# Kernel optimization log

Hardware: AMD Instinct MI355X
Metric: run time of the kernel (lower is better)

## Reference

```python
import jax, jax.numpy as jnp
import numpy as np

D = 128        # d_model
B = 32         # graphs in batch
NV = 500       # vars per graph -> 2*NV literals per graph
NL = B * 2 * NV            # 32000 literals
NC_G = 2000                # clauses per graph
NC = B * NC_G              # 64000 clauses
K = 3                      # literals per clause
NE = NC * K                # 192000 edges


def setup_inputs() -> dict:
    key = jax.random.key(0)
    ks = jax.random.split(key, 16)
    s = 1.0 / np.sqrt(D)
    inp = {
        'x_unk': jax.random.uniform(ks[0], (NL, D), dtype=jnp.float32),
        'C_w': jax.random.normal(ks[1], (D,), dtype=jnp.float32) * s,
        'C_b': jax.random.normal(ks[2], (D,), dtype=jnp.float32) * s,
        'Wih_lc': jax.random.normal(ks[3], (4 * D, D), dtype=jnp.float32) * s,
        'Whh_lc': jax.random.normal(ks[4], (4 * D, D), dtype=jnp.float32) * s,
        'bih_lc': jax.random.normal(ks[5], (4 * D,), dtype=jnp.float32) * s,
        'bhh_lc': jax.random.normal(ks[6], (4 * D,), dtype=jnp.float32) * s,
        'Wih_cl': jax.random.normal(ks[7], (4 * D, 2 * D), dtype=jnp.float32) * s,
        'Whh_cl': jax.random.normal(ks[8], (4 * D, D), dtype=jnp.float32) * s,
        'bih_cl': jax.random.normal(ks[9], (4 * D,), dtype=jnp.float32) * s,
        'bhh_cl': jax.random.normal(ks[10], (4 * D,), dtype=jnp.float32) * s,
        'out_w': jax.random.normal(ks[11], (D, 1), dtype=jnp.float32) * s,
        'out_b': jax.random.normal(ks[12], (1,), dtype=jnp.float32) * s,
    }
    rng = np.random.default_rng(0)
    # each clause samples K literals within its own graph
    lit_local = rng.integers(0, 2 * NV, size=(B, NC_G, K))
    offs = (np.arange(B) * 2 * NV)[:, None, None]
    inp['lit_idx'] = jnp.asarray((lit_local + offs).reshape(-1), dtype=jnp.int32)
    inp['clause_idx'] = jnp.asarray(np.repeat(np.arange(NC), K), dtype=jnp.int32)
    inp['l_batch'] = jnp.asarray(np.repeat(np.arange(B), 2 * NV), dtype=jnp.int32)
    # literal flip: swap pos/neg halves within each graph
    loc = np.arange(2 * NV)
    flip_local = np.concatenate([loc[NV:], loc[:NV]])
    inp['flip_perm'] = jnp.asarray(((np.arange(B) * 2 * NV)[:, None] + flip_local[None, :]).reshape(-1), dtype=jnp.int32)
    inp['num_iters'] = 4
    return inp


def _lstm_step(x, h, c, Wih, Whh, bih, bhh):
    # PyTorch LSTM cell: gates ordered [i, f, g, o]
    g = x @ Wih.T + h @ Whh.T + (bih + bhh)
    i, f, gg, o = jnp.split(g, 4, axis=-1)
    c2 = jax.nn.sigmoid(f) * c + jax.nn.sigmoid(i) * jnp.tanh(gg)
    h2 = jax.nn.sigmoid(o) * jnp.tanh(c2)
    return h2, c2


def reference(x_unk, C_w, C_b, Wih_lc, Whh_lc, bih_lc, bhh_lc,
              Wih_cl, Whh_cl, bih_cl, bhh_cl, out_w, out_b,
              clause_idx, lit_idx, l_batch, flip_perm, num_iters):
    n_lits = x_unk.shape[0]
    n_clauses = clause_idx.shape[0] // K
    # init embeddings: x_unk ~ U[0,1); x_c = C_init(1) repeated; cell states zero
    h_l, c_l = x_unk, jnp.zeros_like(x_unk)
    h_c = jnp.broadcast_to(C_w + C_b, (n_clauses, D))  # Linear(1,d) on ones(1)
    c_c = jnp.zeros((n_clauses, D), dtype=x_unk.dtype)
    for _ in range(num_iters):
        # lit -> clause: msg = adj_t @ x_l (SpMM via gather+segment_sum)
        msg_c = jax.ops.segment_sum(h_l[lit_idx], clause_idx, num_segments=n_clauses)
        h_c, c_c = _lstm_step(msg_c, h_c, c_c, Wih_lc, Whh_lc, bih_lc, bhh_lc)
        # clause -> lit: msg = adj_t.T @ x_c, concat with flipped literals
        msg_l = jax.ops.segment_sum(h_c[clause_idx], lit_idx, num_segments=n_lits)
        inp = jnp.concatenate([msg_l, h_l[flip_perm]], axis=-1)  # [NL, 2D]
        h_l, c_l = _lstm_step(inp, h_l, c_l, Wih_cl, Whh_cl, bih_cl, bhh_cl)
    votes = h_l @ out_w + out_b  # [NL, 1]
    sums = jax.ops.segment_sum(votes, l_batch, num_segments=B)
    cnts = jax.ops.segment_sum(jnp.ones((n_lits, 1), votes.dtype), l_batch, num_segments=B)
    vote_reduced = sums / cnts  # global_mean_pool
    return vote_reduced, votes, h_l
```

## Files before the change

kernel.cpp:

```cpp
#include <hip/hip_runtime.h>
#include <hip/hip_bf16.h>

#define D     128
#define NLIT  32000
#define NCLA  64000
#define KLIT  3
#define NEDGE 192000
#define BGR   32
#define ITERS 4
#define LITS_PER_GRAPH 1000

typedef _Float16 f16x8 __attribute__((ext_vector_type(8)));
typedef float    f32x4 __attribute__((ext_vector_type(4)));

#define TSTRIDE 40

__device__ __forceinline__ float sigf(float x)  { return 1.f / (1.f + __expf(-x)); }
__device__ __forceinline__ float tanhft(float x){ return 1.f - 2.f / (__expf(2.f * x) + 1.f); }

__global__ void conv_x_kernel(const float* __restrict__ x, _Float16* __restrict__ o) {
    int t = blockIdx.x * blockDim.x + threadIdx.x;
    if (t >= NLIT * 16) return;
    const float* p = x + t * 8;
    f16x8 v;
#pragma unroll
    for (int i = 0; i < 8; ++i) v[i] = (_Float16)p[i];
    *(f16x8*)((_Float16*)o + t * 8) = v;
}

__global__ void conv_wc_kernel(const float* __restrict__ Wih,
                               const float* __restrict__ Whh,
                               _Float16* __restrict__ Wc) {
    int n = blockIdx.x, k = threadIdx.x;
    float v = (k < 128) ? Wih[n * 128 + k] : Whh[n * 128 + k - 128];
    Wc[n * 256 + k] = (_Float16)v;
}

__global__ void conv_wl_kernel(const float* __restrict__ Wih,
                               const float* __restrict__ Whh,
                               _Float16* __restrict__ Wl) {
    int n = blockIdx.x, k = threadIdx.x;
    float v = (k < 256) ? Wih[n * 256 + k] : Whh[n * 128 + k - 256];
    Wl[n * 384 + k] = (_Float16)v;
}

__global__ void conv_bias_kernel(const float* bih_c, const float* bhh_c, float* bc,
                                 const float* bih_l, const float* bhh_l, float* bl,
                                 const float* C_w, const float* C_b,
                                 _Float16* hc0g) {
    int t = threadIdx.x;
    bc[t] = bih_c[t] + bhh_c[t];
    bl[t] = bih_l[t] + bhh_l[t];
    if (t < 128) hc0g[t] = (_Float16)(C_w[t] + C_b[t]);
}

__global__ void count_edges_kernel(const int* __restrict__ lit_idx,
                                   int* __restrict__ counts) {
    int e = blockIdx.x * blockDim.x + threadIdx.x;
    if (e < NEDGE) atomicAdd(&counts[lit_idx[e]], 1);
}

__global__ __launch_bounds__(256)
void block_sum_kernel(const int* __restrict__ counts, int* __restrict__ bsum) {
    int b = blockIdx.x, t = threadIdx.x;
    int v = counts[b * 256 + t];
    int lane = t & 63, w = t >> 6;
#pragma unroll
    for (int off = 32; off > 0; off >>= 1) v += __shfl_down(v, off, 64);
    __shared__ int ws[4];
    if (lane == 0) ws[w] = v;
    __syncthreads();
    if (t == 0) bsum[b] = ws[0] + ws[1] + ws[2] + ws[3];
}

__global__ void scan_bsum_kernel(const int* __restrict__ bsum,
                                 int* __restrict__ ebsum,
                                 int* __restrict__ starts) {
    __shared__ int s[128];
    int t = threadIdx.x;
    int v = (t < 125) ? bsum[t] : 0;
    s[t] = v;
    __syncthreads();
    for (int off = 1; off < 128; off <<= 1) {
        int y = (t >= off) ? s[t - off] : 0;
        __syncthreads();
        s[t] += y;
        __syncthreads();
    }
    if (t < 125) ebsum[t] = s[t] - v;
    if (t == 0) starts[NLIT] = NEDGE;
}

__global__ __launch_bounds__(256)
void scan_write_kernel(const int* __restrict__ counts,
                       const int* __restrict__ ebsum,
                       int* __restrict__ starts,
                       int* __restrict__ cursor) {
    int b = blockIdx.x, t = threadIdx.x;
    int idx = b * 256 + t;
    int v = counts[idx];
    int lane = t & 63, w = t >> 6;
    int x = v;
#pragma unroll
    for (int off = 1; off < 64; off <<= 1) {
        int y = __shfl_up(x, off, 64);
        if (lane >= off) x += y;
    }
    __shared__ int wsum[4];
    if (lane == 63) wsum[w] = x;
    __syncthreads();
    int woff = 0;
#pragma unroll
    for (int i = 0; i < 4; ++i) if (i < w) woff += wsum[i];
    int g = ebsum[b] + woff + x - v;
    starts[idx] = g;
    cursor[idx] = g;
}

__global__ void fill_csr_kernel(const int* __restrict__ lit_idx,
                                const int* __restrict__ clause_idx,
                                int* __restrict__ cursor,
                                int* __restrict__ edge_clause) {
    int e = blockIdx.x * blockDim.x + threadIdx.x;
    if (e < NEDGE) {
        int l = lit_idx[e];
        int pos = atomicAdd(&cursor[l], 1);
        edge_clause[pos] = clause_idx[e];
    }
}

__global__ void gather_msg_kernel(const _Float16* __restrict__ h_c16,
                                  _Float16* __restrict__ msg16,
                                  const int* __restrict__ starts,
                                  const int* __restrict__ edge_clause) {
    int t = blockIdx.x * blockDim.x + threadIdx.x;
    if (t >= NLIT * 16) return;
    int l = t >> 4;
    int off = (t & 15) * 8;
    int s = starts[l], e = starts[l + 1];
    float a[8];
#pragma unroll
    for (int i = 0; i < 8; ++i) a[i] = 0.f;
    for (int j = s; j < e; ++j) {
        f16x8 v = *(const f16x8*)&h_c16[(size_t)edge_clause[j] * D + off];
#pragma unroll
        for (int i = 0; i < 8; ++i) a[i] += (float)v[i];
    }
    f16x8 o;
#pragma unroll
    for (int i = 0; i < 8; ++i) o[i] = (_Float16)a[i];
    *(f16x8*)&msg16[(size_t)l * D + off] = o;
}

__global__ __launch_bounds__(256, 3)
void clause_mfma_kernel(const _Float16* __restrict__ h_l16,
                        const _Float16* __restrict__ h_c_old,
                        _Float16* __restrict__ h_c_new,
                        _Float16* __restrict__ c_c16,
                        const _Float16* __restrict__ Wc,
                        const float* __restrict__ bc,
                        const _Float16* __restrict__ hc0g,
                        const int* __restrict__ lit_idx,
                        int first) {
    __shared__ _Float16 At[2][64 * TSTRIDE];
    __shared__ int      lidx[192];

    const int tid  = threadIdx.x;
    const int w    = tid >> 6;
    const int lane = tid & 63;
    const int qd   = lane >> 4;
    const int ln   = lane & 15;
    const int c    = blockIdx.x & 1;
    const int row0 = (blockIdx.x >> 1) * 64;

    if (tid < 192) lidx[tid] = lit_idx[row0 * 3 + tid];
    __syncthreads();

    const int nrow = c * 64 + 16 * w + ln;
    const int koff = qd * 8;
    const int m    = tid >> 2;
    const int col8 = (tid & 3) * 8;

    const _Float16* p0 = &h_l16[(size_t)lidx[3 * m + 0] * D + col8];
    const _Float16* p1 = &h_l16[(size_t)lidx[3 * m + 1] * D + col8];
    const _Float16* p2 = &h_l16[(size_t)lidx[3 * m + 2] * D + col8];
    const _Float16* pc = &h_c_old[(size_t)(row0 + m) * D + col8];
    const _Float16* pb0 = &Wc[(size_t)(0 * 128 + nrow) * 256 + koff];
    const _Float16* pb1 = &Wc[(size_t)(1 * 128 + nrow) * 256 + koff];
    const _Float16* pb2 = &Wc[(size_t)(2 * 128 + nrow) * 256 + koff];
    const _Float16* pb3 = &Wc[(size_t)(3 * 128 + nrow) * 256 + koff];

    f16x8 ldB0 = *(const f16x8*)pb0; pb0 += 32;
    f16x8 ldB1 = *(const f16x8*)pb1; pb1 += 32;
    f16x8 ldB2 = *(const f16x8*)pb2; pb2 += 32;
    f16x8 ldB3 = *(const f16x8*)pb3; pb3 += 32;
    f16x8 ldG0 = *(const f16x8*)p0;  p0 += 32;
    f16x8 ldG1 = *(const f16x8*)p1;  p1 += 32;
    f16x8 ldG2 = *(const f16x8*)p2;  p2 += 32;

    f32x4 acc[4][4];
#pragma unroll
    for (int R = 0; R < 4; ++R)
#pragma unroll
        for (int g = 0; g < 4; ++g) { acc[R][g][0]=0.f; acc[R][g][1]=0.f; acc[R][g][2]=0.f; acc[R][g][3]=0.f; }

    for (int ch = 0; ch < 8; ++ch) {
        _Float16* buf = (_Float16*)At[ch & 1];
        f16x8 o = (ch < 4) ? (f16x8)(ldG0 + ldG1 + ldG2) : ldG0;
        *(f16x8*)&buf[m * TSTRIDE + col8] = o;
        f16x8 bf0 = ldB0, bf1 = ldB1, bf2 = ldB2, bf3 = ldB3;
        if (ch < 7) {
            ldB0 = *(const f16x8*)pb0; pb0 += 32;
            ldB1 = *(const f16x8*)pb1; pb1 += 32;
            ldB2 = *(const f16x8*)pb2; pb2 += 32;
            ldB3 = *(const f16x8*)pb3; pb3 += 32;
            if (ch + 1 < 4) {
                ldG0 = *(const f16x8*)p0; p0 += 32;
                ldG1 = *(const f16x8*)p1; p1 += 32;
                ldG2 = *(const f16x8*)p2; p2 += 32;
            } else if (first) {
                ldG0 = *(const f16x8*)&hc0g[(ch + 1 - 4) * 32 + col8];
            } else {
                ldG0 = *(const f16x8*)pc; pc += 32;
            }
        }
        __syncthreads();
        f16x8 af[4];
#pragma unroll
        for (int R = 0; R < 4; ++R)
            af[R] = *(const f16x8*)&buf[(16 * R + ln) * TSTRIDE + koff];
#pragma unroll
        for (int R = 0; R < 4; ++R) {
            acc[R][0] = __builtin_amdgcn_mfma_f32_16x16x32_f16(af[R], bf0, acc[R][0], 0, 0, 0);
            acc[R][1] = __builtin_amdgcn_mfma_f32_16x16x32_f16(af[R], bf1, acc[R][1], 0, 0, 0);
            acc[R][2] = __builtin_amdgcn_mfma_f32_16x16x32_f16(af[R], bf2, acc[R][2], 0, 0, 0);
            acc[R][3] = __builtin_amdgcn_mfma_f32_16x16x32_f16(af[R], bf3, acc[R][3], 0, 0, 0);
        }
    }

    const int dcol = c * 64 + 16 * w + ln;
    const float b0 = bc[dcol], b1 = bc[128 + dcol], b2 = bc[256 + dcol], b3 = bc[384 + dcol];
#pragma unroll
    for (int R = 0; R < 4; ++R) {
#pragma unroll
        for (int r = 0; r < 4; ++r) {
            int mm = row0 + 16 * R + qd * 4 + r;
            size_t idx = (size_t)mm * D + dcol;
            float gi = acc[R][0][r] + b0;
            float gf = acc[R][1][r] + b1;
            float gg = acc[R][2][r] + b2;
            float go = acc[R][3][r] + b3;
            float cn = sigf(gi) * tanhft(gg);
            if (!first) cn += sigf(gf) * (float)c_c16[idx];
            float h  = sigf(go) * tanhft(cn);
            c_c16[idx]   = (_Float16)cn;
            h_c_new[idx] = (_Float16)h;
        }
    }
}

__global__ __launch_bounds__(256, 3)
void literal_mfma_kernel(const _Float16* __restrict__ h_old16,
                         const _Float16* __restrict__ msg16,
                         _Float16* __restrict__ h_new16,
                         float* __restrict__ h32,
                         _Float16* __restrict__ c_l16,
                         const _Float16* __restrict__ Wl384,
                         const float* __restrict__ bl,
                         const int* __restrict__ flip_perm,
                         int first) {
    __shared__ _Float16 At[2][64 * TSTRIDE];
    __shared__ int      flip_s[64];

    const int tid  = threadIdx.x;
    const int w    = tid >> 6;
    const int lane = tid & 63;
    const int qd   = lane >> 4;
    const int ln   = lane & 15;
    const int c    = blockIdx.x & 1;
    const int row0 = (blockIdx.x >> 1) * 64;

    if (tid < 64) flip_s[tid] = flip_perm[row0 + tid];
    __syncthreads();

    const int nrow = c * 64 + 16 * w + ln;
    const int koff = qd * 8;
    const int m    = tid >> 2;
    const int col8 = (tid & 3) * 8;

    const _Float16* pf = &h_old16[(size_t)flip_s[m] * D + col8];
    const _Float16* po = &h_old16[(size_t)(row0 + m) * D + col8];
    const _Float16* cur = &msg16[(size_t)(row0 + m) * D + col8];
    const _Float16* pb0 = &Wl384[(size_t)(0 * 128 + nrow) * 384 + koff];
    const _Float16* pb1 = &Wl384[(size_t)(1 * 128 + nrow) * 384 + koff];
    const _Float16* pb2 = &Wl384[(size_t)(2 * 128 + nrow) * 384 + koff];
    const _Float16* pb3 = &Wl384[(size_t)(3 * 128 + nrow) * 384 + koff];

    f16x8 ldB0 = *(const f16x8*)pb0; pb0 += 32;
    f16x8 ldB1 = *(const f16x8*)pb1; pb1 += 32;
    f16x8 ldB2 = *(const f16x8*)pb2; pb2 += 32;
    f16x8 ldB3 = *(const f16x8*)pb3; pb3 += 32;
    f16x8 ldA  = *(const f16x8*)cur; cur += 32;

    f32x4 acc[4][4];
#pragma unroll
    for (int R = 0; R < 4; ++R)
#pragma unroll
        for (int g = 0; g < 4; ++g) { acc[R][g][0]=0.f; acc[R][g][1]=0.f; acc[R][g][2]=0.f; acc[R][g][3]=0.f; }

    for (int ch = 0; ch < 12; ++ch) {
        _Float16* buf = (_Float16*)At[ch & 1];
        *(f16x8*)&buf[m * TSTRIDE + col8] = ldA;
        f16x8 bf0 = ldB0, bf1 = ldB1, bf2 = ldB2, bf3 = ldB3;
        if (ch < 11) {
            ldB0 = *(const f16x8*)pb0; pb0 += 32;
            ldB1 = *(const f16x8*)pb1; pb1 += 32;
            ldB2 = *(const f16x8*)pb2; pb2 += 32;
            ldB3 = *(const f16x8*)pb3; pb3 += 32;
            if (ch + 1 == 4)      cur = pf;
            else if (ch + 1 == 8) cur = po;
            ldA = *(const f16x8*)cur; cur += 32;
        }
        __syncthreads();
        f16x8 af[4];
#pragma unroll
        for (int R = 0; R < 4; ++R)
            af[R] = *(const f16x8*)&buf[(16 * R + ln) * TSTRIDE + koff];
#pragma unroll
        for (int R = 0; R < 4; ++R) {
            acc[R][0] = __builtin_amdgcn_mfma_f32_16x16x32_f16(af[R], bf0, acc[R][0], 0, 0, 0);
            acc[R][1] = __builtin_amdgcn_mfma_f32_16x16x32_f16(af[R], bf1, acc[R][1], 0, 0, 0);
            acc[R][2] = __builtin_amdgcn_mfma_f32_16x16x32_f16(af[R], bf2, acc[R][2], 0, 0, 0);
            acc[R][3] = __builtin_amdgcn_mfma_f32_16x16x32_f16(af[R], bf3, acc[R][3], 0, 0, 0);
        }
    }

    const int dcol = c * 64 + 16 * w + ln;
    const float b0 = bl[dcol], b1 = bl[128 + dcol], b2 = bl[256 + dcol], b3 = bl[384 + dcol];
#pragma unroll
    for (int R = 0; R < 4; ++R) {
#pragma unroll
        for (int r = 0; r < 4; ++r) {
            int mm = row0 + 16 * R + qd * 4 + r;
            size_t idx = (size_t)mm * D + dcol;
            float gi = acc[R][0][r] + b0;
            float gf = acc[R][1][r] + b1;
            float gg = acc[R][2][r] + b2;
            float go = acc[R][3][r] + b3;
            float cn = sigf(gi) * tanhft(gg);
            if (!first) cn += sigf(gf) * (float)c_l16[idx];
            float h  = sigf(go) * tanhft(cn);
            c_l16[idx]   = (_Float16)cn;
            h_new16[idx] = (_Float16)h;
            if (h32) h32[idx] = h;
        }
    }
}

__global__ __launch_bounds__(256)
void votes_stage1_kernel(const float* __restrict__ h_l,
                         const float* __restrict__ out_w,
                         const float* __restrict__ out_b,
                         float* __restrict__ votes_out) {
    int w    = threadIdx.x >> 6;
    int lane = threadIdx.x & 63;
    int l    = blockIdx.x * 4 + w;
    if (l >= NLIT) return;
    const float2 v = *(const float2*)&h_l[(size_t)l * D + lane * 2];
    const float2 ww = *(const float2*)&out_w[lane * 2];
    float p = v.x * ww.x + v.y * ww.y;
#pragma unroll
    for (int off = 32; off > 0; off >>= 1) p += __shfl_down(p, off, 64);
    if (lane == 0) votes_out[l] = p + out_b[0];
}

__global__ __launch_bounds__(256)
void votes_stage2_kernel(const float* __restrict__ votes,
                         float* __restrict__ out0) {
    int b = blockIdx.x;
    int t = threadIdx.x;
    const float* base = votes + (size_t)b * LITS_PER_GRAPH;
    float s = 0.f;
    for (int i = t; i < LITS_PER_GRAPH; i += 256) s += base[i];
#pragma unroll
    for (int off = 32; off > 0; off >>= 1) s += __shfl_down(s, off, 64);
    __shared__ float ws[4];
    if ((t & 63) == 0) ws[t >> 6] = s;
    __syncthreads();
    if (t == 0) out0[b] = (ws[0] + ws[1] + ws[2] + ws[3]) / (float)LITS_PER_GRAPH;
}

extern "C" void kernel_launch(void* const* d_in, const int* in_sizes, int n_in,
                              void* d_out, int out_size, void* d_ws, size_t ws_size,
                              hipStream_t stream) {
    (void)in_sizes; (void)n_in; (void)out_size; (void)ws_size;

    const float* x_unk  = (const float*)d_in[0];
    const float* C_w    = (const float*)d_in[1];
    const float* C_b    = (const float*)d_in[2];
    const float* Wih_lc = (const float*)d_in[3];
    const float* Whh_lc = (const float*)d_in[4];
    const float* bih_lc = (const float*)d_in[5];
    const float* bhh_lc = (const float*)d_in[6];
    const float* Wih_cl = (const float*)d_in[7];
    const float* Whh_cl = (const float*)d_in[8];
    const float* bih_cl = (const float*)d_in[9];
    const float* bhh_cl = (const float*)d_in[10];
    const float* out_w  = (const float*)d_in[11];
    const float* out_b  = (const float*)d_in[12];
    const int* lit_idx    = (const int*)d_in[13];
    const int* clause_idx = (const int*)d_in[14];
    const int* flip_perm  = (const int*)d_in[16];

    char* W = (char*)d_ws;
    size_t off = 0;
    auto alloc = [&](size_t bytes) { char* p = W + off; off = (off + bytes + 255) & ~(size_t)255; return p; };
    _Float16* h_l16_0 = (_Float16*)alloc((size_t)NLIT * D * 2);
    _Float16* h_l16_1 = (_Float16*)alloc((size_t)NLIT * D * 2);
    _Float16* h_c16_0 = (_Float16*)alloc((size_t)NCLA * D * 2);
    _Float16* h_c16_1 = (_Float16*)alloc((size_t)NCLA * D * 2);
    _Float16* msg16   = (_Float16*)alloc((size_t)NLIT * D * 2);
    _Float16* c_l16   = (_Float16*)alloc((size_t)NLIT * D * 2);
    _Float16* c_c16   = (_Float16*)alloc((size_t)NCLA * D * 2);
    _Float16* Wc16    = (_Float16*)alloc(512 * 256 * 2);
    _Float16* Wl16    = (_Float16*)alloc(512 * 384 * 2);
    float*    bc      = (float*)  alloc(512 * 4);
    float*    bl      = (float*)  alloc(512 * 4);
    _Float16* hc0g    = (_Float16*)alloc(128 * 2);
    int* counts       = (int*)alloc((size_t)NLIT * 4);
    int* starts       = (int*)alloc((size_t)(NLIT + 1) * 4);
    int* cursor       = (int*)alloc((size_t)NLIT * 4);
    int* edge_clause  = (int*)alloc((size_t)NEDGE * 4);
    int* bsum         = (int*)alloc(128 * 4);
    int* ebsum        = (int*)alloc(128 * 4);

    float* out       = (float*)d_out;
    float* out_votes = out + BGR;
    float* out_hl    = out + BGR + NLIT;

    hipMemsetAsync(counts, 0, (size_t)NLIT * 4, stream);

    conv_x_kernel<<<(NLIT * 16 + 255) / 256, 256, 0, stream>>>(x_unk, h_l16_0);
    conv_wc_kernel<<<512, 256, 0, stream>>>(Wih_lc, Whh_lc, Wc16);
    conv_wl_kernel<<<512, 384, 0, stream>>>(Wih_cl, Whh_cl, Wl16);
    conv_bias_kernel<<<1, 512, 0, stream>>>(bih_lc, bhh_lc, bc, bih_cl, bhh_cl, bl,
                                            C_w, C_b, hc0g);

    count_edges_kernel<<<(NEDGE + 255) / 256, 256, 0, stream>>>(lit_idx, counts);
    block_sum_kernel<<<NLIT / 256, 256, 0, stream>>>(counts, bsum);
    scan_bsum_kernel<<<1, 128, 0, stream>>>(bsum, ebsum, starts);
    scan_write_kernel<<<NLIT / 256, 256, 0, stream>>>(counts, ebsum, starts, cursor);
    fill_csr_kernel<<<(NEDGE + 255) / 256, 256, 0, stream>>>(lit_idx, clause_idx,
                                                             cursor, edge_clause);

    const _Float16* hl_old[ITERS] = {h_l16_0, h_l16_1, h_l16_0, h_l16_1};
    _Float16*       hl_new[ITERS] = {h_l16_1, h_l16_0, h_l16_1, h_l16_0};
    const _Float16* hc_old[ITERS] = {h_c16_0, h_c16_1, h_c16_0, h_c16_1};
    _Float16*       hc_new[ITERS] = {h_c16_1, h_c16_0, h_c16_1, h_c16_0};

    for (int it = 0; it < ITERS; ++it) {
        clause_mfma_kernel<<<(NCLA / 64) * 2, 256, 0, stream>>>(
            hl_old[it], hc_old[it], hc_new[it], c_c16, Wc16, bc, hc0g, lit_idx,
            it == 0 ? 1 : 0);
        gather_msg_kernel<<<(NLIT * 16 + 255) / 256, 256, 0, stream>>>(
            hc_new[it], msg16, starts, edge_clause);
        literal_mfma_kernel<<<(NLIT / 64) * 2, 256, 0, stream>>>(
            hl_old[it], msg16, hl_new[it],
            (it == ITERS - 1) ? out_hl : (float*)nullptr,
            c_l16, Wl16, bl, flip_perm,
            it == 0 ? 1 : 0);
    }

    votes_stage1_kernel<<<NLIT / 4, 256, 0, stream>>>(out_hl, out_w, out_b, out_votes);
    votes_stage2_kernel<<<BGR, 256, 0, stream>>>(out_votes, out);
}
```

Baseline: 548.9 us.

## Drop LDS staging in LSTM MFMA kernels; pre-pack weights into MFMA fragment order

```diff
diff --git a/kernel.cpp b/kernel.cpp
--- a/kernel.cpp
+++ b/kernel.cpp
@@ -13,8 +13,6 @@
 typedef _Float16 f16x8 __attribute__((ext_vector_type(8)));
 typedef float    f32x4 __attribute__((ext_vector_type(4)));
 
-#define TSTRIDE 40
-
 __device__ __forceinline__ float sigf(float x)  { return 1.f / (1.f + __expf(-x)); }
 __device__ __forceinline__ float tanhft(float x){ return 1.f - 2.f / (__expf(2.f * x) + 1.f); }
 
@@ -30,18 +28,24 @@
 
 __global__ void conv_wc_kernel(const float* __restrict__ Wih,
                                const float* __restrict__ Whh,
-                               _Float16* __restrict__ Wc) {
+                               _Float16* __restrict__ WcP) {
     int n = blockIdx.x, k = threadIdx.x;
     float v = (k < 128) ? Wih[n * 128 + k] : Whh[n * 128 + k - 128];
-    Wc[n * 256 + k] = (_Float16)v;
+    int g = n >> 7, rem = n & 127, c = rem >> 6, dt = (rem >> 4) & 3, ln = rem & 15;
+    int ch = k >> 5, qd = (k >> 3) & 3, j = k & 7;
+    size_t off = (((((size_t)ch * 4 + qd) * 2 + c) * 16 + ln) * 16 + (g * 4 + dt)) * 8 + j;
+    WcP[off] = (_Float16)v;
 }
 
 __global__ void conv_wl_kernel(const float* __restrict__ Wih,
                                const float* __restrict__ Whh,
-                               _Float16* __restrict__ Wl) {
+                               _Float16* __restrict__ WlP) {
     int n = blockIdx.x, k = threadIdx.x;
     float v = (k < 256) ? Wih[n * 256 + k] : Whh[n * 128 + k - 256];
-    Wl[n * 384 + k] = (_Float16)v;
+    int g = n >> 7, rem = n & 127, c = rem >> 6, dt = (rem >> 4) & 3, ln = rem & 15;
+    int ch = k >> 5, qd = (k >> 3) & 3, j = k & 7;
+    size_t off = (((((size_t)ch * 4 + qd) * 2 + c) * 16 + ln) * 16 + (g * 4 + dt)) * 8 + j;
+    WlP[off] = (_Float16)v;
 }
 
 __global__ void conv_bias_kernel(const float* bih_c, const float* bhh_c, float* bc,
@@ -157,99 +161,65 @@
                         const _Float16* __restrict__ h_c_old,
                         _Float16* __restrict__ h_c_new,
                         _Float16* __restrict__ c_c16,
-                        const _Float16* __restrict__ Wc,
+                        const _Float16* __restrict__ WcP,
                         const float* __restrict__ bc,
                         const _Float16* __restrict__ hc0g,
                         const int* __restrict__ lit_idx,
                         int first) {
-    __shared__ _Float16 At[2][64 * TSTRIDE];
-    __shared__ int      lidx[192];
-
     const int tid  = threadIdx.x;
     const int w    = tid >> 6;
     const int lane = tid & 63;
     const int qd   = lane >> 4;
     const int ln   = lane & 15;
-    const int c    = blockIdx.x & 1;
-    const int row0 = (blockIdx.x >> 1) * 64;
-
-    if (tid < 192) lidx[tid] = lit_idx[row0 * 3 + tid];
-    __syncthreads();
-
-    const int nrow = c * 64 + 16 * w + ln;
-    const int koff = qd * 8;
-    const int m    = tid >> 2;
-    const int col8 = (tid & 3) * 8;
-
-    const _Float16* p0 = &h_l16[(size_t)lidx[3 * m + 0] * D + col8];
-    const _Float16* p1 = &h_l16[(size_t)lidx[3 * m + 1] * D + col8];
-    const _Float16* p2 = &h_l16[(size_t)lidx[3 * m + 2] * D + col8];
-    const _Float16* pc = &h_c_old[(size_t)(row0 + m) * D + col8];
-    const _Float16* pb0 = &Wc[(size_t)(0 * 128 + nrow) * 256 + koff];
-    const _Float16* pb1 = &Wc[(size_t)(1 * 128 + nrow) * 256 + koff];
-    const _Float16* pb2 = &Wc[(size_t)(2 * 128 + nrow) * 256 + koff];
-    const _Float16* pb3 = &Wc[(size_t)(3 * 128 + nrow) * 256 + koff];
-
-    f16x8 ldB0 = *(const f16x8*)pb0; pb0 += 32;
-    f16x8 ldB1 = *(const f16x8*)pb1; pb1 += 32;
-    f16x8 ldB2 = *(const f16x8*)pb2; pb2 += 32;
-    f16x8 ldB3 = *(const f16x8*)pb3; pb3 += 32;
-    f16x8 ldG0 = *(const f16x8*)p0;  p0 += 32;
-    f16x8 ldG1 = *(const f16x8*)p1;  p1 += 32;
-    f16x8 ldG2 = *(const f16x8*)p2;  p2 += 32;
-
-    f32x4 acc[4][4];
-#pragma unroll
-    for (int R = 0; R < 4; ++R)
-#pragma unroll
-        for (int g = 0; g < 4; ++g) { acc[R][g][0]=0.f; acc[R][g][1]=0.f; acc[R][g][2]=0.f; acc[R][g][3]=0.f; }
-
+    const int c    = (blockIdx.x >= (NCLA / 64)) ? 1 : 0;
+    const int row0 = (blockIdx.x - c * (NCLA / 64)) * 64;
+    const int gm   = row0 + 16 * w + ln;
+
+    const int b3 = 3 * gm;
+    const int li0 = lit_idx[b3 + 0], li1 = lit_idx[b3 + 1], li2 = lit_idx[b3 + 2];
+    const _Float16* pa0 = h_l16 + (size_t)li0 * D + qd * 8;
+    const _Float16* pa1 = h_l16 + (size_t)li1 * D + qd * 8;
+    const _Float16* pa2 = h_l16 + (size_t)li2 * D + qd * 8;
+    const _Float16* pcc = first ? (hc0g + qd * 8)
+                                : (h_c_old + (size_t)gm * D + qd * 8);
+
+    const _Float16* pb = WcP + ((((size_t)qd * 2 + c) * 16 + ln) * 128);
+
+    f32x4 acc[16];
+#pragma unroll
+    for (int t = 0; t < 16; ++t) { acc[t][0]=0.f; acc[t][1]=0.f; acc[t][2]=0.f; acc[t][3]=0.f; }
+
+#pragma unroll
     for (int ch = 0; ch < 8; ++ch) {
-        _Float16* buf = (_Float16*)At[ch & 1];
-        f16x8 o = (ch < 4) ? (f16x8)(ldG0 + ldG1 + ldG2) : ldG0;
-        *(f16x8*)&buf[m * TSTRIDE + col8] = o;
-        f16x8 bf0 = ldB0, bf1 = ldB1, bf2 = ldB2, bf3 = ldB3;
-        if (ch < 7) {
-            ldB0 = *(const f16x8*)pb0; pb0 += 32;
-            ldB1 = *(const f16x8*)pb1; pb1 += 32;
-            ldB2 = *(const f16x8*)pb2; pb2 += 32;
-            ldB3 = *(const f16x8*)pb3; pb3 += 32;
-            if (ch + 1 < 4) {
-                ldG0 = *(const f16x8*)p0; p0 += 32;
-                ldG1 = *(const f16x8*)p1; p1 += 32;
-                ldG2 = *(const f16x8*)p2; p2 += 32;
-            } else if (first) {
-                ldG0 = *(const f16x8*)&hc0g[(ch + 1 - 4) * 32 + col8];
-            } else {
-                ldG0 = *(const f16x8*)pc; pc += 32;
-            }
+        f16x8 af;
+        if (ch < 4) {
+            f16x8 a0 = *(const f16x8*)(pa0 + ch * 32);
+            f16x8 a1 = *(const f16x8*)(pa1 + ch * 32);
+            f16x8 a2 = *(const f16x8*)(pa2 + ch * 32);
+            af = a0 + a1 + a2;
+        } else {
+            af = *(const f16x8*)(pcc + (ch - 4) * 32);
         }
-        __syncthreads();
-        f16x8 af[4];
-#pragma unroll
-        for (int R = 0; R < 4; ++R)
-            af[R] = *(const f16x8*)&buf[(16 * R + ln) * TSTRIDE + koff];
-#pragma unroll
-        for (int R = 0; R < 4; ++R) {
-            acc[R][0] = __builtin_amdgcn_mfma_f32_16x16x32_f16(af[R], bf0, acc[R][0], 0, 0, 0);
-            acc[R][1] = __builtin_amdgcn_mfma_f32_16x16x32_f16(af[R], bf1, acc[R][1], 0, 0, 0);
-            acc[R][2] = __builtin_amdgcn_mfma_f32_16x16x32_f16(af[R], bf2, acc[R][2], 0, 0, 0);
-            acc[R][3] = __builtin_amdgcn_mfma_f32_16x16x32_f16(af[R], bf3, acc[R][3], 0, 0, 0);
+        const _Float16* pbc = pb + (size_t)ch * 16384;
+#pragma unroll
+        for (int t = 0; t < 16; ++t) {
+            f16x8 bf = *(const f16x8*)(pbc + t * 8);
+            acc[t] = __builtin_amdgcn_mfma_f32_16x16x32_f16(af, bf, acc[t], 0, 0, 0);
         }
     }
 
-    const int dcol = c * 64 + 16 * w + ln;
-    const float b0 = bc[dcol], b1 = bc[128 + dcol], b2 = bc[256 + dcol], b3 = bc[384 + dcol];
-#pragma unroll
-    for (int R = 0; R < 4; ++R) {
+#pragma unroll
+    for (int dt = 0; dt < 4; ++dt) {
+        const int dcol = c * 64 + dt * 16 + ln;
+        const float b0 = bc[dcol], b1 = bc[128 + dcol], b2 = bc[256 + dcol], b3f = bc[384 + dcol];
 #pragma unroll
         for (int r = 0; r < 4; ++r) {
-            int mm = row0 + 16 * R + qd * 4 + r;
-            size_t idx = (size_t)mm * D + dcol;
-            float gi = acc[R][0][r] + b0;
-            float gf = acc[R][1][r] + b1;
-            float gg = acc[R][2][r] + b2;
-            float go = acc[R][3][r] + b3;
+            int m = row0 + 16 * w + qd * 4 + r;
+            size_t idx = (size_t)m * D + dcol;
+            float gi = acc[0 * 4 + dt][r] + b0;
+            float gf = acc[1 * 4 + dt][r] + b1;
+            float gg = acc[2 * 4 + dt][r] + b2;
+            float go = acc[3 * 4 + dt][r] + b3f;
             float cn = sigf(gi) * tanhft(gg);
             if (!first) cn += sigf(gf) * (float)c_c16[idx];
             float h  = sigf(go) * tanhft(cn);
@@ -265,88 +235,56 @@
                          _Float16* __restrict__ h_new16,
                          float* __restrict__ h32,
                          _Float16* __restrict__ c_l16,
-                         const _Float16* __restrict__ Wl384,
+                         const _Float16* __restrict__ WlP,
                          const float* __restrict__ bl,
                          const int* __restrict__ flip_perm,
                          int first) {
-    __shared__ _Float16 At[2][64 * TSTRIDE];
-    __shared__ int      flip_s[64];
-
     const int tid  = threadIdx.x;
     const int w    = tid >> 6;
     const int lane = tid & 63;
     const int qd   = lane >> 4;
     const int ln   = lane & 15;
-    const int c    = blockIdx.x & 1;
-    const int row0 = (blockIdx.x >> 1) * 64;
-
-    if (tid < 64) flip_s[tid] = flip_perm[row0 + tid];
-    __syncthreads();
-
-    const int nrow = c * 64 + 16 * w + ln;
-    const int koff = qd * 8;
-    const int m    = tid >> 2;
-    const int col8 = (tid & 3) * 8;
-
-    const _Float16* pf = &h_old16[(size_t)flip_s[m] * D + col8];
-    const _Float16* po = &h_old16[(size_t)(row0 + m) * D + col8];
-    const _Float16* cur = &msg16[(size_t)(row0 + m) * D + col8];
-    const _Float16* pb0 = &Wl384[(size_t)(0 * 128 + nrow) * 384 + koff];
-    const _Float16* pb1 = &Wl384[(size_t)(1 * 128 + nrow) * 384 + koff];
-    const _Float16* pb2 = &Wl384[(size_t)(2 * 128 + nrow) * 384 + koff];
-    const _Float16* pb3 = &Wl384[(size_t)(3 * 128 + nrow) * 384 + koff];
-
-    f16x8 ldB0 = *(const f16x8*)pb0; pb0 += 32;
-    f16x8 ldB1 = *(const f16x8*)pb1; pb1 += 32;
-    f16x8 ldB2 = *(const f16x8*)pb2; pb2 += 32;
-    f16x8 ldB3 = *(const f16x8*)pb3; pb3 += 32;
-    f16x8 ldA  = *(const f16x8*)cur; cur += 32;
-
-    f32x4 acc[4][4];
-#pragma unroll
-    for (int R = 0; R < 4; ++R)
-#pragma unroll
-        for (int g = 0; g < 4; ++g) { acc[R][g][0]=0.f; acc[R][g][1]=0.f; acc[R][g][2]=0.f; acc[R][g][3]=0.f; }
-
+    const int c    = (blockIdx.x >= (NLIT / 64)) ? 1 : 0;
+    const int row0 = (blockIdx.x - c * (NLIT / 64)) * 64;
+    const int gm   = row0 + 16 * w + ln;
+
+    const int fl = flip_perm[gm];
+    const _Float16* pm = msg16   + (size_t)gm * D + qd * 8;
+    const _Float16* pf = h_old16 + (size_t)fl * D + qd * 8;
+    const _Float16* po = h_old16 + (size_t)gm * D + qd * 8;
+
+    const _Float16* pb = WlP + ((((size_t)qd * 2 + c) * 16 + ln) * 128);
+
+    f32x4 acc[16];
+#pragma unroll
+    for (int t = 0; t < 16; ++t) { acc[t][0]=0.f; acc[t][1]=0.f; acc[t][2]=0.f; acc[t][3]=0.f; }
+
+#pragma unroll
     for (int ch = 0; ch < 12; ++ch) {
-        _Float16* buf = (_Float16*)At[ch & 1];
-        *(f16x8*)&buf[m * TSTRIDE + col8] = ldA;
-        f16x8 bf0 = ldB0, bf1 = ldB1, bf2 = ldB2, bf3 = ldB3;
-        if (ch < 11) {
-            ldB0 = *(const f16x8*)pb0; pb0 += 32;
-            ldB1 = *(const f16x8*)pb1; pb1 += 32;
-            ldB2 = *(const f16x8*)pb2; pb2 += 32;
-            ldB3 = *(const f16x8*)pb3; pb3 += 32;
-            if (ch + 1 == 4)      cur = pf;
-            else if (ch + 1 == 8) cur = po;
-            ldA = *(const f16x8*)cur; cur += 32;
+        f16x8 af;
+        if (ch < 4)      af = *(const f16x8*)(pm + ch * 32);
+        else if (ch < 8) af = *(const f16x8*)(pf + (ch - 4) * 32);
+        else             af = *(const f16x8*)(po + (ch - 8) * 32);
+        const _Float16* pbc = pb + (size_t)ch * 16384;
+#pragma unroll
+        for (int t = 0; t < 16; ++t) {
+            f16x8 bf = *(const f16x8*)(pbc + t * 8);
+            acc[t] = __builtin_amdgcn_mfma_f32_16x16x32_f16(af, bf, acc[t], 0, 0, 0);
         }
-        __syncthreads();
-        f16x8 af[4];
-#pragma unroll
-        for (int R = 0; R < 4; ++R)
-            af[R] = *(const f16x8*)&buf[(16 * R + ln) * TSTRIDE + koff];
-#pragma unroll
-        for (int R = 0; R < 4; ++R) {
-            acc[R][0] = __builtin_amdgcn_mfma_f32_16x16x32_f16(af[R], bf0, acc[R][0], 0, 0, 0);
-            acc[R][1] = __builtin_amdgcn_mfma_f32_16x16x32_f16(af[R], bf1, acc[R][1], 0, 0, 0);
-            acc[R][2] = __builtin_amdgcn_mfma_f32_16x16x32_f16(af[R], bf2, acc[R][2], 0, 0, 0);
-            acc[R][3] = __builtin_amdgcn_mfma_f32_16x16x32_f16(af[R], bf3, acc[R][3], 0, 0, 0);
-        }
-    }
-
-    const int dcol = c * 64 + 16 * w + ln;
-    const float b0 = bl[dcol], b1 = bl[128 + dcol], b2 = bl[256 + dcol], b3 = bl[384 + dcol];
-#pragma unroll
-    for (int R = 0; R < 4; ++R) {
+    }
+
+#pragma unroll
+    for (int dt = 0; dt < 4; ++dt) {
+        const int dcol = c * 64 + dt * 16 + ln;
+        const float b0 = bl[dcol], b1 = bl[128 + dcol], b2 = bl[256 + dcol], b3f = bl[384 + dcol];
 #pragma unroll
         for (int r = 0; r < 4; ++r) {
-            int mm = row0 + 16 * R + qd * 4 + r;
-            size_t idx = (size_t)mm * D + dcol;
-            float gi = acc[R][0][r] + b0;
-            float gf = acc[R][1][r] + b1;
-            float gg = acc[R][2][r] + b2;
-            float go = acc[R][3][r] + b3;
+            int m = row0 + 16 * w + qd * 4 + r;
+            size_t idx = (size_t)m * D + dcol;
+            float gi = acc[0 * 4 + dt][r] + b0;
+            float gf = acc[1 * 4 + dt][r] + b1;
+            float gg = acc[2 * 4 + dt][r] + b2;
+            float go = acc[3 * 4 + dt][r] + b3f;
             float cn = sigf(gi) * tanhft(gg);
             if (!first) cn += sigf(gf) * (float)c_l16[idx];
             float h  = sigf(go) * tanhft(cn);
```

New measurement: 1.177 ms. +114.3%, slower.

## Merge column-half blocks into 512-thread blocks with prepacked weights and blob cell state

Applied to the files above, without the earlier changes.

```diff
diff --git a/kernel.cpp b/kernel.cpp
--- a/kernel.cpp
+++ b/kernel.cpp
@@ -30,18 +30,24 @@
 
 __global__ void conv_wc_kernel(const float* __restrict__ Wih,
                                const float* __restrict__ Whh,
-                               _Float16* __restrict__ Wc) {
+                               _Float16* __restrict__ WcP) {
     int n = blockIdx.x, k = threadIdx.x;
     float v = (k < 128) ? Wih[n * 128 + k] : Whh[n * 128 + k - 128];
-    Wc[n * 256 + k] = (_Float16)v;
+    int g = n >> 7, dcol = n & 127;
+    int ch = k >> 5, qd = (k >> 3) & 3, j = k & 7;
+    size_t off = ((((size_t)ch * 4 + qd) * 128 + dcol) * 4 + g) * 8 + j;
+    WcP[off] = (_Float16)v;
 }
 
 __global__ void conv_wl_kernel(const float* __restrict__ Wih,
                                const float* __restrict__ Whh,
-                               _Float16* __restrict__ Wl) {
+                               _Float16* __restrict__ WlP) {
     int n = blockIdx.x, k = threadIdx.x;
     float v = (k < 256) ? Wih[n * 256 + k] : Whh[n * 128 + k - 256];
-    Wl[n * 384 + k] = (_Float16)v;
+    int g = n >> 7, dcol = n & 127;
+    int ch = k >> 5, qd = (k >> 3) & 3, j = k & 7;
+    size_t off = ((((size_t)ch * 4 + qd) * 128 + dcol) * 4 + g) * 8 + j;
+    WlP[off] = (_Float16)v;
 }
 
 __global__ void conv_bias_kernel(const float* bih_c, const float* bhh_c, float* bc,
@@ -152,51 +158,49 @@
     *(f16x8*)&msg16[(size_t)l * D + off] = o;
 }
 
-__global__ __launch_bounds__(256, 3)
+__global__ __launch_bounds__(512, 3)
 void clause_mfma_kernel(const _Float16* __restrict__ h_l16,
                         const _Float16* __restrict__ h_c_old,
                         _Float16* __restrict__ h_c_new,
-                        _Float16* __restrict__ c_c16,
-                        const _Float16* __restrict__ Wc,
+                        _Float16* __restrict__ c_blob,
+                        const _Float16* __restrict__ WcP,
                         const float* __restrict__ bc,
                         const _Float16* __restrict__ hc0g,
                         const int* __restrict__ lit_idx,
                         int first) {
     __shared__ _Float16 At[2][64 * TSTRIDE];
-    __shared__ int      lidx[192];
 
     const int tid  = threadIdx.x;
     const int w    = tid >> 6;
     const int lane = tid & 63;
     const int qd   = lane >> 4;
     const int ln   = lane & 15;
-    const int c    = blockIdx.x & 1;
-    const int row0 = (blockIdx.x >> 1) * 64;
-
-    if (tid < 192) lidx[tid] = lit_idx[row0 * 3 + tid];
-    __syncthreads();
-
-    const int nrow = c * 64 + 16 * w + ln;
-    const int koff = qd * 8;
+    const int row0 = blockIdx.x * 64;
+    const int dcol = 16 * w + ln;
+
+    const _Float16* pb = WcP + ((size_t)qd * 128 + dcol) * 32;
+
     const int m    = tid >> 2;
     const int col8 = (tid & 3) * 8;
-
-    const _Float16* p0 = &h_l16[(size_t)lidx[3 * m + 0] * D + col8];
-    const _Float16* p1 = &h_l16[(size_t)lidx[3 * m + 1] * D + col8];
-    const _Float16* p2 = &h_l16[(size_t)lidx[3 * m + 2] * D + col8];
-    const _Float16* pc = &h_c_old[(size_t)(row0 + m) * D + col8];
-    const _Float16* pb0 = &Wc[(size_t)(0 * 128 + nrow) * 256 + koff];
-    const _Float16* pb1 = &Wc[(size_t)(1 * 128 + nrow) * 256 + koff];
-    const _Float16* pb2 = &Wc[(size_t)(2 * 128 + nrow) * 256 + koff];
-    const _Float16* pb3 = &Wc[(size_t)(3 * 128 + nrow) * 256 + koff];
-
-    f16x8 ldB0 = *(const f16x8*)pb0; pb0 += 32;
-    f16x8 ldB1 = *(const f16x8*)pb1; pb1 += 32;
-    f16x8 ldB2 = *(const f16x8*)pb2; pb2 += 32;
-    f16x8 ldB3 = *(const f16x8*)pb3; pb3 += 32;
-    f16x8 ldG0 = *(const f16x8*)p0;  p0 += 32;
-    f16x8 ldG1 = *(const f16x8*)p1;  p1 += 32;
-    f16x8 ldG2 = *(const f16x8*)p2;  p2 += 32;
+    const _Float16 *pa0 = nullptr, *pa1 = nullptr, *pa2 = nullptr, *pcc = nullptr;
+    if (tid < 256) {
+        int b3 = 3 * (row0 + m);
+        pa0 = h_l16 + (size_t)lit_idx[b3 + 0] * D + col8;
+        pa1 = h_l16 + (size_t)lit_idx[b3 + 1] * D + col8;
+        pa2 = h_l16 + (size_t)lit_idx[b3 + 2] * D + col8;
+        pcc = first ? (hc0g + col8) : (h_c_old + (size_t)(row0 + m) * D + col8);
+    }
+
+    f16x8 ldB0, ldB1, ldB2, ldB3, ldG0, ldG1, ldG2;
+    ldB0 = *(const f16x8*)(pb + 0);
+    ldB1 = *(const f16x8*)(pb + 8);
+    ldB2 = *(const f16x8*)(pb + 16);
+    ldB3 = *(const f16x8*)(pb + 24);
+    if (tid < 256) {
+        ldG0 = *(const f16x8*)pa0; pa0 += 32;
+        ldG1 = *(const f16x8*)pa1; pa1 += 32;
+        ldG2 = *(const f16x8*)pa2; pa2 += 32;
+    }
 
     f32x4 acc[4][4];
 #pragma unroll
@@ -206,29 +210,34 @@
 
     for (int ch = 0; ch < 8; ++ch) {
         _Float16* buf = (_Float16*)At[ch & 1];
-        f16x8 o = (ch < 4) ? (f16x8)(ldG0 + ldG1 + ldG2) : ldG0;
-        *(f16x8*)&buf[m * TSTRIDE + col8] = o;
+        if (tid < 256) {
+            f16x8 o = (ch < 4) ? (f16x8)(ldG0 + ldG1 + ldG2) : ldG0;
+            *(f16x8*)&buf[m * TSTRIDE + col8] = o;
+        }
         f16x8 bf0 = ldB0, bf1 = ldB1, bf2 = ldB2, bf3 = ldB3;
         if (ch < 7) {
-            ldB0 = *(const f16x8*)pb0; pb0 += 32;
-            ldB1 = *(const f16x8*)pb1; pb1 += 32;
-            ldB2 = *(const f16x8*)pb2; pb2 += 32;
-            ldB3 = *(const f16x8*)pb3; pb3 += 32;
-            if (ch + 1 < 4) {
-                ldG0 = *(const f16x8*)p0; p0 += 32;
-                ldG1 = *(const f16x8*)p1; p1 += 32;
-                ldG2 = *(const f16x8*)p2; p2 += 32;
-            } else if (first) {
-                ldG0 = *(const f16x8*)&hc0g[(ch + 1 - 4) * 32 + col8];
-            } else {
-                ldG0 = *(const f16x8*)pc; pc += 32;
+            const _Float16* pbn = pb + (size_t)(ch + 1) * 16384;
+            ldB0 = *(const f16x8*)(pbn + 0);
+            ldB1 = *(const f16x8*)(pbn + 8);
+            ldB2 = *(const f16x8*)(pbn + 16);
+            ldB3 = *(const f16x8*)(pbn + 24);
+            if (tid < 256) {
+                if (ch + 1 < 4) {
+                    ldG0 = *(const f16x8*)pa0; pa0 += 32;
+                    ldG1 = *(const f16x8*)pa1; pa1 += 32;
+                    ldG2 = *(const f16x8*)pa2; pa2 += 32;
+                } else if (first) {
+                    ldG0 = *(const f16x8*)(hc0g + (ch + 1 - 4) * 32 + col8);
+                } else {
+                    ldG0 = *(const f16x8*)pcc; pcc += 32;
+                }
             }
         }
         __syncthreads();
         f16x8 af[4];
 #pragma unroll
         for (int R = 0; R < 4; ++R)
-            af[R] = *(const f16x8*)&buf[(16 * R + ln) * TSTRIDE + koff];
+            af[R] = *(const f16x8*)&buf[(16 * R + ln) * TSTRIDE + qd * 8];
 #pragma unroll
         for (int R = 0; R < 4; ++R) {
             acc[R][0] = __builtin_amdgcn_mfma_f32_16x16x32_f16(af[R], bf0, acc[R][0], 0, 0, 0);
@@ -238,123 +247,132 @@
         }
     }
 
-    const int dcol = c * 64 + 16 * w + ln;
-    const float b0 = bc[dcol], b1 = bc[128 + dcol], b2 = bc[256 + dcol], b3 = bc[384 + dcol];
+    _Float16* cb = c_blob + ((size_t)blockIdx.x * 512 + tid) * 16;
+    f16x8 cold0, cold1;
+    if (!first) { cold0 = *(const f16x8*)cb; cold1 = *(const f16x8*)(cb + 8); }
+    const float b0 = bc[dcol], b1 = bc[128 + dcol], b2 = bc[256 + dcol], b3f = bc[384 + dcol];
+    f16x8 cnew0, cnew1;
 #pragma unroll
     for (int R = 0; R < 4; ++R) {
 #pragma unroll
         for (int r = 0; r < 4; ++r) {
+            int i = R * 4 + r;
+            int mm = row0 + 16 * R + qd * 4 + r;
+            float gi = acc[R][0][r] + b0;
+            float gf = acc[R][1][r] + b1;
+            float gg = acc[R][2][r] + b2;
+            float go = acc[R][3][r] + b3f;
+            float cn = sigf(gi) * tanhft(gg);
+            if (!first) cn += sigf(gf) * (float)((i < 8) ? cold0[i & 7] : cold1[i & 7]);
+            float h  = sigf(go) * tanhft(cn);
+            if (i < 8) cnew0[i & 7] = (_Float16)cn; else cnew1[i & 7] = (_Float16)cn;
+            h_c_new[(size_t)mm * D + dcol] = (_Float16)h;
+        }
+    }
+    *(f16x8*)cb = cnew0;
+    *(f16x8*)(cb + 8) = cnew1;
+}
+
+__global__ __launch_bounds__(512, 3)
+void literal_mfma_kernel(const _Float16* __restrict__ h_old16,
+                         const _Float16* __restrict__ msg16,
+                         _Float16* __restrict__ h_new16,
+                         float* __restrict__ h32,
+                         _Float16* __restrict__ c_blob,
+                         const _Float16* __restrict__ WlP,
+                         const float* __restrict__ bl,
+                         const int* __restrict__ flip_perm,
+                         int first) {
+    __shared__ _Float16 At[2][64 * TSTRIDE];
+
+    const int tid  = threadIdx.x;
+    const int w    = tid >> 6;
+    const int lane = tid & 63;
+    const int qd   = lane >> 4;
+    const int ln   = lane & 15;
+    const int row0 = blockIdx.x * 64;
+    const int dcol = 16 * w + ln;
+
+    const _Float16* pb = WlP + ((size_t)qd * 128 + dcol) * 32;
+
+    const int m    = tid >> 2;
+    const int col8 = (tid & 3) * 8;
+    const _Float16 *cur = nullptr, *pf = nullptr, *po = nullptr;
+    if (tid < 256) {
+        pf  = h_old16 + (size_t)flip_perm[row0 + m] * D + col8;
+        po  = h_old16 + (size_t)(row0 + m) * D + col8;
+        cur = msg16   + (size_t)(row0 + m) * D + col8;
+    }
+
+    f16x8 ldB0, ldB1, ldB2, ldB3, ldA;
+    ldB0 = *(const f16x8*)(pb + 0);
+    ldB1 = *(const f16x8*)(pb + 8);
+    ldB2 = *(const f16x8*)(pb + 16);
+    ldB3 = *(const f16x8*)(pb + 24);
+    if (tid < 256) { ldA = *(const f16x8*)cur; cur += 32; }
+
+    f32x4 acc[4][4];
+#pragma unroll
+    for (int R = 0; R < 4; ++R)
+#pragma unroll
+        for (int g = 0; g < 4; ++g) { acc[R][g][0]=0.f; acc[R][g][1]=0.f; acc[R][g][2]=0.f; acc[R][g][3]=0.f; }
+
+    for (int ch = 0; ch < 12; ++ch) {
+        _Float16* buf = (_Float16*)At[ch & 1];
+        if (tid < 256) *(f16x8*)&buf[m * TSTRIDE + col8] = ldA;
+        f16x8 bf0 = ldB0, bf1 = ldB1, bf2 = ldB2, bf3 = ldB3;
+        if (ch < 11) {
+            const _Float16* pbn = pb + (size_t)(ch + 1) * 16384;
+            ldB0 = *(const f16x8*)(pbn + 0);
+            ldB1 = *(const f16x8*)(pbn + 8);
+            ldB2 = *(const f16x8*)(pbn + 16);
+            ldB3 = *(const f16x8*)(pbn + 24);
+            if (tid < 256) {
+                if (ch + 1 == 4)      cur = pf;
+                else if (ch + 1 == 8) cur = po;
+                ldA = *(const f16x8*)cur; cur += 32;
+            }
+        }
+        __syncthreads();
+        f16x8 af[4];
+#pragma unroll
+        for (int R = 0; R < 4; ++R)
+            af[R] = *(const f16x8*)&buf[(16 * R + ln) * TSTRIDE + qd * 8];
+#pragma unroll
+        for (int R = 0; R < 4; ++R) {
+            acc[R][0] = __builtin_amdgcn_mfma_f32_16x16x32_f16(af[R], bf0, acc[R][0], 0, 0, 0);
+            acc[R][1] = __builtin_amdgcn_mfma_f32_16x16x32_f16(af[R], bf1, acc[R][1], 0, 0, 0);
+            acc[R][2] = __builtin_amdgcn_mfma_f32_16x16x32_f16(af[R], bf2, acc[R][2], 0, 0, 0);
+            acc[R][3] = __builtin_amdgcn_mfma_f32_16x16x32_f16(af[R], bf3, acc[R][3], 0, 0, 0);
+        }
+    }
+
+    _Float16* cb = c_blob + ((size_t)blockIdx.x * 512 + tid) * 16;
+    f16x8 cold0, cold1;
+    if (!first) { cold0 = *(const f16x8*)cb; cold1 = *(const f16x8*)(cb + 8); }
+    const float b0 = bl[dcol], b1 = bl[128 + dcol], b2 = bl[256 + dcol], b3f = bl[384 + dcol];
+    f16x8 cnew0, cnew1;
+#pragma unroll
+    for (int R = 0; R < 4; ++R) {
+#pragma unroll
+        for (int r = 0; r < 4; ++r) {
+            int i = R * 4 + r;
             int mm = row0 + 16 * R + qd * 4 + r;
             size_t idx = (size_t)mm * D + dcol;
             float gi = acc[R][0][r] + b0;
             float gf = acc[R][1][r] + b1;
             float gg = acc[R][2][r] + b2;
-            float go = acc[R][3][r] + b3;
+            float go = acc[R][3][r] + b3f;
             float cn = sigf(gi) * tanhft(gg);
-            if (!first) cn += sigf(gf) * (float)c_c16[idx];
+            if (!first) cn += sigf(gf) * (float)((i < 8) ? cold0[i & 7] : cold1[i & 7]);
             float h  = sigf(go) * tanhft(cn);
-            c_c16[idx]   = (_Float16)cn;
-            h_c_new[idx] = (_Float16)h;
-        }
-    }
-}
-
-__global__ __launch_bounds__(256, 3)
-void literal_mfma_kernel(const _Float16* __restrict__ h_old16,
-                         const _Float16* __restrict__ msg16,
-                         _Float16* __restrict__ h_new16,
-                         float* __restrict__ h32,
-                         _Float16* __restrict__ c_l16,
-                         const _Float16* __restrict__ Wl384,
-                         const float* __restrict__ bl,
-                         const int* __restrict__ flip_perm,
-                         int first) {
-    __shared__ _Float16 At[2][64 * TSTRIDE];
-    __shared__ int      flip_s[64];
-
-    const int tid  = threadIdx.x;
-    const int w    = tid >> 6;
-    const int lane = tid & 63;
-    const int qd   = lane >> 4;
-    const int ln   = lane & 15;
-    const int c    = blockIdx.x & 1;
-    const int row0 = (blockIdx.x >> 1) * 64;
-
-    if (tid < 64) flip_s[tid] = flip_perm[row0 + tid];
-    __syncthreads();
-
-    const int nrow = c * 64 + 16 * w + ln;
-    const int koff = qd * 8;
-    const int m    = tid >> 2;
-    const int col8 = (tid & 3) * 8;
-
-    const _Float16* pf = &h_old16[(size_t)flip_s[m] * D + col8];
-    const _Float16* po = &h_old16[(size_t)(row0 + m) * D + col8];
-    const _Float16* cur = &msg16[(size_t)(row0 + m) * D + col8];
-    const _Float16* pb0 = &Wl384[(size_t)(0 * 128 + nrow) * 384 + koff];
-    const _Float16* pb1 = &Wl384[(size_t)(1 * 128 + nrow) * 384 + koff];
-    const _Float16* pb2 = &Wl384[(size_t)(2 * 128 + nrow) * 384 + koff];
-    const _Float16* pb3 = &Wl384[(size_t)(3 * 128 + nrow) * 384 + koff];
-
-    f16x8 ldB0 = *(const f16x8*)pb0; pb0 += 32;
-    f16x8 ldB1 = *(const f16x8*)pb1; pb1 += 32;
-    f16x8 ldB2 = *(const f16x8*)pb2; pb2 += 32;
-    f16x8 ldB3 = *(const f16x8*)pb3; pb3 += 32;
-    f16x8 ldA  = *(const f16x8*)cur; cur += 32;
-
-    f32x4 acc[4][4];
-#pragma unroll
-    for (int R = 0; R < 4; ++R)
-#pragma unroll
-        for (int g = 0; g < 4; ++g) { acc[R][g][0]=0.f; acc[R][g][1]=0.f; acc[R][g][2]=0.f; acc[R][g][3]=0.f; }
-
-    for (int ch = 0; ch < 12; ++ch) {
-        _Float16* buf = (_Float16*)At[ch & 1];
-        *(f16x8*)&buf[m * TSTRIDE + col8] = ldA;
-        f16x8 bf0 = ldB0, bf1 = ldB1, bf2 = ldB2, bf3 = ldB3;
-        if (ch < 11) {
-            ldB0 = *(const f16x8*)pb0; pb0 += 32;
-            ldB1 = *(const f16x8*)pb1; pb1 += 32;
-            ldB2 = *(const f16x8*)pb2; pb2 += 32;
-            ldB3 = *(const f16x8*)pb3; pb3 += 32;
-            if (ch + 1 == 4)      cur = pf;
-            else if (ch + 1 == 8) cur = po;
-            ldA = *(const f16x8*)cur; cur += 32;
-        }
-        __syncthreads();
-        f16x8 af[4];
-#pragma unroll
-        for (int R = 0; R < 4; ++R)
-            af[R] = *(const f16x8*)&buf[(16 * R + ln) * TSTRIDE + koff];
-#pragma unroll
-        for (int R = 0; R < 4; ++R) {
-            acc[R][0] = __builtin_amdgcn_mfma_f32_16x16x32_f16(af[R], bf0, acc[R][0], 0, 0, 0);
-            acc[R][1] = __builtin_amdgcn_mfma_f32_16x16x32_f16(af[R], bf1, acc[R][1], 0, 0, 0);
-            acc[R][2] = __builtin_amdgcn_mfma_f32_16x16x32_f16(af[R], bf2, acc[R][2], 0, 0, 0);
-            acc[R][3] = __builtin_amdgcn_mfma_f32_16x16x32_f16(af[R], bf3, acc[R][3], 0, 0, 0);
-        }
-    }
-
-    const int dcol = c * 64 + 16 * w + ln;
-    const float b0 = bl[dcol], b1 = bl[128 + dcol], b2 = bl[256 + dcol], b3 = bl[384 + dcol];
-#pragma unroll
-    for (int R = 0; R < 4; ++R) {
-#pragma unroll
-        for (int r = 0; r < 4; ++r) {
-            int mm = row0 + 16 * R + qd * 4 + r;
-            size_t idx = (size_t)mm * D + dcol;
-            float gi = acc[R][0][r] + b0;
-            float gf = acc[R][1][r] + b1;
-            float gg = acc[R][2][r] + b2;
-            float go = acc[R][3][r] + b3;
-            float cn = sigf(gi) * tanhft(gg);
-            if (!first) cn += sigf(gf) * (float)c_l16[idx];
-            float h  = sigf(go) * tanhft(cn);
-            c_l16[idx]   = (_Float16)cn;
+            if (i < 8) cnew0[i & 7] = (_Float16)cn; else cnew1[i & 7] = (_Float16)cn;
             h_new16[idx] = (_Float16)h;
             if (h32) h32[idx] = h;
         }
     }
+    *(f16x8*)cb = cnew0;
+    *(f16x8*)(cb + 8) = cnew1;
 }
 
 __global__ __launch_bounds__(256)
@@ -459,12 +477,12 @@
     _Float16*       hc_new[ITERS] = {h_c16_1, h_c16_0, h_c16_1, h_c16_0};
 
     for (int it = 0; it < ITERS; ++it) {
-        clause_mfma_kernel<<<(NCLA / 64) * 2, 256, 0, stream>>>(
+        clause_mfma_kernel<<<NCLA / 64, 512, 0, stream>>>(
             hl_old[it], hc_old[it], hc_new[it], c_c16, Wc16, bc, hc0g, lit_idx,
             it == 0 ? 1 : 0);
         gather_msg_kernel<<<(NLIT * 16 + 255) / 256, 256, 0, stream>>>(
             hc_new[it], msg16, starts, edge_clause);
-        literal_mfma_kernel<<<(NLIT / 64) * 2, 256, 0, stream>>>(
+        literal_mfma_kernel<<<NLIT / 64, 512, 0, stream>>>(
             hl_old[it], msg16, hl_new[it],
             (it == ITERS - 1) ? out_hl : (float*)nullptr,
             c_l16, Wl16, bl, flip_perm,
```

New measurement: 464.7 us. 1.18x faster.
